# Optimization experiments

Hardware: AMD Instinct MI355X
Metric: run time of the kernel (lower is better)

The kernel has to match this reference:

```python
import jax, jax.numpy as jnp
import numpy as np

B, H, W = 16, 384, 1280
HW = H * W
K = 131072  # number of top-k selected pixels per batch element


def setup_inputs() -> dict:
    key = jax.random.key(0)
    k1, k2, k3 = jax.random.split(key, 3)
    # depth map in a plausible metric range
    depth = jax.random.uniform(k1, (B, 1, H, W), jnp.float32, 0.1, 80.0)
    inv_K = jax.random.normal(k2, (B, 4, 4), jnp.float32)
    top_k_indices = jax.random.randint(k3, (B, K), 0, HW)
    # non-trainable buffer: homogeneous pixel coordinates [B, 3, HW]
    gx, gy = np.meshgrid(np.arange(W), np.arange(H), indexing='xy')
    pix = np.stack([gx.reshape(-1), gy.reshape(-1), np.ones(HW)], axis=0).astype(np.float32)  # [3, HW]
    pix_coords = jnp.tile(jnp.asarray(pix)[None], (B, 1, 1))  # [B, 3, HW]
    return {"depth": depth, "inv_K": inv_K, "pix_coords": pix_coords,
            "top_k_indices": top_k_indices}


def reference(depth, inv_K, pix_coords, top_k_indices):
    b, k = top_k_indices.shape
    idx1 = top_k_indices[:, None, :]                      # [B, 1, K]
    idx3 = jnp.broadcast_to(idx1, (b, 3, k))              # [B, 3, K]
    # gather selected homogeneous pixel coords -> [B, 3, K]
    pix_sel = jnp.take_along_axis(pix_coords, idx3, axis=2)
    # small batched 3x3 matmul: rays in camera frame
    cam_points = jnp.einsum('bij,bjk->bik', inv_K[:, :3, :3], pix_sel)  # [B, 3, K]
    # gather selected depths -> [B, 1, K]
    depth_flat = depth.reshape(b, 1, -1)
    depth_sel = jnp.take_along_axis(depth_flat, idx1, axis=2)
    cam_points = depth_sel * cam_points
    ones_sel = jnp.ones_like(depth_sel)                   # ones buffer gather is all ones
    return jnp.concatenate([cam_points, ones_sel], axis=1)  # [B, 4, K]
```

## Files before the change

### kernel.cpp

```cpp
#include <hip/hip_runtime.h>


#define BB 16
#define HH 384
#define WW 1280
#define HWSZ (HH * WW)
#define HW4 (HWSZ / 4)
#define KK 131072
#define NXCD 8
#define BLOCKS_PER_BATCH (KK / (256 * 4))
#define TOTAL_BLOCKS (BB * BLOCKS_PER_BATCH)
#define WARM_F4_PER_BLOCK (HW4 / BLOCKS_PER_BATCH)

typedef float v4f __attribute__((ext_vector_type(4)));
typedef int   v4i __attribute__((ext_vector_type(4)));

__device__ __forceinline__ void xcd_map(int bid, int& b, int& blk) {
    const int xcd  = bid & (NXCD - 1);
    const int slot = bid >> 3;
    const int logical = xcd * (TOTAL_BLOCKS / NXCD) + slot;
    b   = logical >> 7;
    blk = logical & 127;
}

__global__ __launch_bounds__(256) void warm_kernel(
    const float* __restrict__ depth, float* __restrict__ out)
{
    int b, blk;
    xcd_map(blockIdx.x, b, blk);

    const v4f* __restrict__ d4 = reinterpret_cast<const v4f*>(depth) + b * HW4;
    float acc = 0.f;
#pragma unroll
    for (int it = 0; it < 4; ++it) {
        const int i = blk * WARM_F4_PER_BLOCK + it * 256 + threadIdx.x;
        if (it < 3 || i < (blk + 1) * WARM_F4_PER_BLOCK) {
            const v4f v = d4[i];
            acc += v[0] + v[1] + v[2] + v[3];
        }
    }
    asm volatile("" :: "v"(acc));

    const int k0 = blk * 1024 + threadIdx.x * 4;
    float* __restrict__ ob = out + (size_t)b * 4 * KK + 3 * KK + k0;
    v4f vw = {1.f, 1.f, 1.f, 1.f};
    __builtin_nontemporal_store(vw, reinterpret_cast<v4f*>(ob));
}

__global__ __launch_bounds__(256) void backproject_kernel(
    const float* __restrict__ depth,
    const float* __restrict__ invK,
    const int*   __restrict__ topk,
    float*       __restrict__ out)
{
    int b, blk;
    xcd_map(blockIdx.x, b, blk);
    const int k0 = blk * 1024 + threadIdx.x * 4;

    const float* __restrict__ M = invK + b * 16;
    const float m00 = M[0], m01 = M[1], m02 = M[2];
    const float m10 = M[4], m11 = M[5], m12 = M[6];
    const float m20 = M[8], m21 = M[9], m22 = M[10];

    const v4i idx4 = __builtin_nontemporal_load(
        reinterpret_cast<const v4i*>(topk + b * KK + k0));
    const float* __restrict__ db = depth + b * HWSZ;

    const int idxs[4] = {idx4[0], idx4[1], idx4[2], idx4[3]};
    float d[4];
#pragma unroll
    for (int j = 0; j < 4; ++j) d[j] = db[idxs[j]];

    float ox[4], oy[4], oz[4];
#pragma unroll
    for (int j = 0; j < 4; ++j) {
        const int idx = idxs[j];
        const float gx = (float)(idx % WW);
        const float gy = (float)(idx / WW);
        ox[j] = d[j] * fmaf(m00, gx, fmaf(m01, gy, m02));
        oy[j] = d[j] * fmaf(m10, gx, fmaf(m11, gy, m12));
        oz[j] = d[j] * fmaf(m20, gx, fmaf(m21, gy, m22));
    }

    float* __restrict__ ob = out + (size_t)b * 4 * KK + k0;
    v4f vx = {ox[0], ox[1], ox[2], ox[3]};
    v4f vy = {oy[0], oy[1], oy[2], oy[3]};
    v4f vz = {oz[0], oz[1], oz[2], oz[3]};
    __builtin_nontemporal_store(vx, reinterpret_cast<v4f*>(ob + 0 * KK));
    __builtin_nontemporal_store(vy, reinterpret_cast<v4f*>(ob + 1 * KK));
    __builtin_nontemporal_store(vz, reinterpret_cast<v4f*>(ob + 2 * KK));
}

extern "C" void kernel_launch(void* const* d_in, const int* in_sizes, int n_in,
                              void* d_out, int out_size, void* d_ws, size_t ws_size,
                              hipStream_t stream) {
    const float* depth = (const float*)d_in[0];
    const float* invK  = (const float*)d_in[1];
    const int*   topk  = (const int*)d_in[3];
    float* out = (float*)d_out;

    warm_kernel<<<TOTAL_BLOCKS, 256, 0, stream>>>(depth, out);
    backproject_kernel<<<TOTAL_BLOCKS, 256, 0, stream>>>(depth, invK, topk, out);
}
```

Before: 22.58 us.

## Fuse depth warm-up streaming and ones-row store into the backprojection kernel

Removes the separate warm kernel and folds its work into the main kernel. Each block now streams its slice of the depth map with coalesced vector loads while the random gathers are in flight, and it also writes the constant ones row. This saves one kernel launch and the gap between the two kernels, and lets the coalesced sweep overlap the gathers. The cost is more registers per thread and more outstanding memory traffic inside one kernel, and the gathers may miss cache because the sweep no longer finishes before them.

```diff
diff --git a/kernel.cpp b/kernel.cpp
--- a/kernel.cpp
+++ b/kernel.cpp
@@ -23,30 +23,6 @@
     blk = logical & 127;
 }
 
-__global__ __launch_bounds__(256) void warm_kernel(
-    const float* __restrict__ depth, float* __restrict__ out)
-{
-    int b, blk;
-    xcd_map(blockIdx.x, b, blk);
-
-    const v4f* __restrict__ d4 = reinterpret_cast<const v4f*>(depth) + b * HW4;
-    float acc = 0.f;
-#pragma unroll
-    for (int it = 0; it < 4; ++it) {
-        const int i = blk * WARM_F4_PER_BLOCK + it * 256 + threadIdx.x;
-        if (it < 3 || i < (blk + 1) * WARM_F4_PER_BLOCK) {
-            const v4f v = d4[i];
-            acc += v[0] + v[1] + v[2] + v[3];
-        }
-    }
-    asm volatile("" :: "v"(acc));
-
-    const int k0 = blk * 1024 + threadIdx.x * 4;
-    float* __restrict__ ob = out + (size_t)b * 4 * KK + 3 * KK + k0;
-    v4f vw = {1.f, 1.f, 1.f, 1.f};
-    __builtin_nontemporal_store(vw, reinterpret_cast<v4f*>(ob));
-}
-
 __global__ __launch_bounds__(256) void backproject_kernel(
     const float* __restrict__ depth,
     const float* __restrict__ invK,
@@ -57,19 +33,29 @@
     xcd_map(blockIdx.x, b, blk);
     const int k0 = blk * 1024 + threadIdx.x * 4;
 
+    const v4i idx4 = __builtin_nontemporal_load(
+        reinterpret_cast<const v4i*>(topk + b * KK + k0));
+
+    const v4f* __restrict__ w4 =
+        reinterpret_cast<const v4f*>(depth) + b * HW4 + blk * WARM_F4_PER_BLOCK;
+    const int t = threadIdx.x;
+    const v4f w0 = w4[t];
+    const v4f w1 = w4[256 + t];
+    const v4f w2 = w4[512 + t];
+    const v4f w3 = w4[768 + (t < 192 ? t : 0)];
+
     const float* __restrict__ M = invK + b * 16;
     const float m00 = M[0], m01 = M[1], m02 = M[2];
     const float m10 = M[4], m11 = M[5], m12 = M[6];
     const float m20 = M[8], m21 = M[9], m22 = M[10];
 
-    const v4i idx4 = __builtin_nontemporal_load(
-        reinterpret_cast<const v4i*>(topk + b * KK + k0));
     const float* __restrict__ db = depth + b * HWSZ;
-
     const int idxs[4] = {idx4[0], idx4[1], idx4[2], idx4[3]};
     float d[4];
 #pragma unroll
     for (int j = 0; j < 4; ++j) d[j] = db[idxs[j]];
+
+    asm volatile("" :: "v"(w0), "v"(w1), "v"(w2), "v"(w3));
 
     float ox[4], oy[4], oz[4];
 #pragma unroll
@@ -86,9 +72,11 @@
     v4f vx = {ox[0], ox[1], ox[2], ox[3]};
     v4f vy = {oy[0], oy[1], oy[2], oy[3]};
     v4f vz = {oz[0], oz[1], oz[2], oz[3]};
+    v4f vw = {1.f, 1.f, 1.f, 1.f};
     __builtin_nontemporal_store(vx, reinterpret_cast<v4f*>(ob + 0 * KK));
     __builtin_nontemporal_store(vy, reinterpret_cast<v4f*>(ob + 1 * KK));
     __builtin_nontemporal_store(vz, reinterpret_cast<v4f*>(ob + 2 * KK));
+    __builtin_nontemporal_store(vw, reinterpret_cast<v4f*>(ob + 3 * KK));
 }
 
 extern "C" void kernel_launch(void* const* d_in, const int* in_sizes, int n_in,
@@ -99,6 +87,5 @@
     const int*   topk  = (const int*)d_in[3];
     float* out = (float*)d_out;
 
-    warm_kernel<<<TOTAL_BLOCKS, 256, 0, stream>>>(depth, out);
     backproject_kernel<<<TOTAL_BLOCKS, 256, 0, stream>>>(depth, invK, topk, out);
 }
```

After: 24.86 us. 10.1% more time.
